# Kernel tuning notes

Measured on AMD Instinct MI355X. Metric: run time of the kernel, lower is better.

## Reference

```python
import jax, jax.numpy as jnp
import numpy as np

L = 32            # fixed label space replacing torch.unique (labels in [0, L))
DELTA_AGG = 0.5
DELTA_DIS = 1.5
REG_W = 0.001


def safe_norm(sq):
    # sqrt with zero-safe gradient: returns 0 where sq == 0
    safe = jnp.where(sq > 0, sq, 1.0)
    return jnp.where(sq > 0, jnp.sqrt(safe), 0.0)


def _single(emb, instance, kernel, training_mask):
    D = emb.shape[0]
    tm = training_mask > 0.5
    kn = kernel > 0.5
    inst = jnp.where(tm, instance, 0).reshape(-1)          # (N,) masked instance labels
    inst_k = jnp.where(tm & kn, instance, 0).reshape(-1)   # (N,) kernel-region labels
    embf = emb.reshape(D, -1).T                            # (N, D)
    ones = jnp.ones(inst.shape, dtype=jnp.float32)

    # per-label kernel means (emb_mean), label 0 stays zero as in torch
    cnt_k = jax.ops.segment_sum(ones, inst_k, num_segments=L)            # (L,)
    sum_k = jax.ops.segment_sum(embf, inst_k, num_segments=L)            # (L, D)
    emb_mean = sum_k / jnp.maximum(cnt_k, 1.0)[:, None]
    emb_mean = emb_mean.at[0].set(0.0)

    present = cnt_k > 0
    num_instance = jnp.sum(present.astype(jnp.int32))
    nz = present & (jnp.arange(L) > 0)

    # aggregation loss: per-pixel distance to own instance's kernel mean
    diff = embf - emb_mean[inst]                                          # (N, D)
    dist = safe_norm(jnp.sum(diff * diff, axis=1))
    val = jnp.log(jax.nn.relu(dist - DELTA_AGG) ** 2 + 1.0)
    sum_v = jax.ops.segment_sum(val, inst, num_segments=L)
    cnt = jax.ops.segment_sum(ones, inst, num_segments=L)
    l_agg_per = sum_v / jnp.maximum(cnt, 1.0)
    l_agg = jnp.sum(jnp.where(nz, l_agg_per, 0.0)) / jnp.maximum(num_instance - 1, 1)

    # discrimination loss: all pairs of distinct non-background present labels
    pdiff = emb_mean[:, None, :] - emb_mean[None, :, :]                   # (L, L, D)
    pdist = safe_norm(jnp.sum(pdiff * pdiff, axis=-1))
    pval = jnp.log(jax.nn.relu(2.0 * DELTA_DIS - pdist) ** 2 + 1.0)
    pmask = nz[:, None] & nz[None, :] & ~jnp.eye(L, dtype=bool)
    n_pairs = jnp.sum(pmask.astype(jnp.float32))
    l_dis = jnp.sum(jnp.where(pmask, pval, 0.0)) / jnp.maximum(n_pairs, 1.0)
    l_dis = jnp.where(num_instance > 2, l_dis, 0.0)

    # regularizer over the num_instance present columns of emb_mean
    reg = jnp.log(safe_norm(jnp.sum(emb_mean * emb_mean, axis=1)) + 1.0)
    l_reg = jnp.sum(jnp.where(present, reg, 0.0)) / jnp.maximum(num_instance, 1) * REG_W

    loss = l_agg + l_dis + l_reg
    return jnp.where(num_instance <= 1, 0.0, loss)


def setup_inputs() -> dict:
    key = jax.random.key(0)
    k1, k2, k3, k4 = jax.random.split(key, 4)
    B, D, H, W = 8, 4, 736, 736
    emb = jax.random.normal(k1, (B, D, H, W), dtype=jnp.float32)
    instance = jax.random.randint(k2, (B, H, W), 0, L, dtype=jnp.int32)
    kernel = jax.random.uniform(k3, (B, H, W), dtype=jnp.float32)
    training_mask = jax.random.uniform(k4, (B, H, W), dtype=jnp.float32)
    return {"emb": emb, "instance": instance, "kernel": kernel, "training_mask": training_mask}


def reference(emb, instance, kernel, training_mask):
    return jax.vmap(_single)(emb, instance, kernel, training_mask)
```

## Files before the change

### kernel.cpp

```cpp
#include <hip/hip_runtime.h>

#define LBL 32
#define NPIX (736 * 736)
#define NQ (NPIX / 4)
#define QPB 512
#define NBA 265
#define BATCH 8
#define DELTA_AGG 0.5f
#define DELTA_DIS 1.5f
#define REG_W 0.001f

#define LAB_BASE 0
#define PA_BASE (BATCH * NQ)
#define RED_BASE (PA_BASE + BATCH * NBA * 192)
#define PC_BASE (RED_BASE + BATCH * 256)

__device__ __forceinline__ unsigned int procQuad(
    const int4 iv, const float4 kv, const float4 mv,
    const float4 e0, const float4 e1, const float4 e2, const float4 e3,
    float* __restrict__ s_cnt, float* __restrict__ s_sum,
    float* __restrict__ s_cta, bool& has0) {
  const int labs[4] = {iv.x, iv.y, iv.z, iv.w};
  const float ks[4] = {kv.x, kv.y, kv.z, kv.w};
  const float ms[4] = {mv.x, mv.y, mv.z, mv.w};
  const float c0[4] = {e0.x, e0.y, e0.z, e0.w};
  const float c1[4] = {e1.x, e1.y, e1.z, e1.w};
  const float c2[4] = {e2.x, e2.y, e2.z, e2.w};
  const float c3[4] = {e3.x, e3.y, e3.z, e3.w};
  unsigned int labw = 0;
#pragma unroll
  for (int j = 0; j < 4; j++) {
    const bool m = ms[j] > 0.5f;
    const int li = m ? labs[j] : 0;
    const bool kf = m && (ks[j] > 0.5f);
    labw |= ((unsigned int)li) << (8 * j);
    if (li > 0) {
      atomicAdd(&s_cta[li], 1.0f);
      if (kf) {
        atomicAdd(&s_cnt[li], 1.0f);
        atomicAdd(&s_sum[0 * 33 + li], c0[j]);
        atomicAdd(&s_sum[1 * 33 + li], c1[j]);
        atomicAdd(&s_sum[2 * 33 + li], c2[j]);
        atomicAdd(&s_sum[3 * 33 + li], c3[j]);
      } else {
        has0 = true;
      }
    } else {
      has0 = true;
    }
  }
  return labw;
}

__global__ __launch_bounds__(256) void kA(
    const float* __restrict__ emb, const int* __restrict__ inst,
    const float* __restrict__ kern, const float* __restrict__ mask,
    float* __restrict__ ws) {
  const int b = blockIdx.y;
  const int t = threadIdx.x;
  __shared__ float s_cnt[LBL];
  __shared__ float s_sum[4 * 33];
  __shared__ float s_cta[LBL];
  if (t < LBL) { s_cnt[t] = 0.f; s_cta[t] = 0.f; }
  if (t < 4 * 33) s_sum[t] = 0.f;
  __syncthreads();

  const long base = (long)b * NPIX;
  const float* ebase = emb + (long)b * 4 * NPIX;
  const int4* ip = (const int4*)(inst + base);
  const float4* kp = (const float4*)(kern + base);
  const float4* mp = (const float4*)(mask + base);
  const float4* p0 = (const float4*)(ebase);
  const float4* p1 = (const float4*)(ebase + NPIX);
  const float4* p2 = (const float4*)(ebase + 2 * NPIX);
  const float4* p3 = (const float4*)(ebase + 3 * NPIX);

  const int q0 = blockIdx.x * QPB + t;
  const int q1 = q0 + 256;
  const bool v1 = (q1 < NQ);

  const int4 iva = ip[q0];
  const float4 kva = kp[q0], mva = mp[q0];
  const float4 ea0 = p0[q0], ea1 = p1[q0], ea2 = p2[q0], ea3 = p3[q0];
  int4 ivb;
  float4 kvb, mvb, fb0, fb1, fb2, fb3;
  if (v1) {
    ivb = ip[q1]; kvb = kp[q1]; mvb = mp[q1];
    fb0 = p0[q1]; fb1 = p1[q1]; fb2 = p2[q1]; fb3 = p3[q1];
  }

  bool has0 = false;
  unsigned int* labp = (unsigned int*)(ws + LAB_BASE) + (size_t)b * NQ;

  labp[q0] = procQuad(iva, kva, mva, ea0, ea1, ea2, ea3,
                      s_cnt, s_sum, s_cta, has0);
  if (v1) {
    labp[q1] = procQuad(ivb, kvb, mvb, fb0, fb1, fb2, fb3,
                        s_cnt, s_sum, s_cta, has0);
  }

  if (has0) s_cnt[0] = 1.0f;
  __syncthreads();
  float* po = ws + PA_BASE + ((size_t)b * NBA + blockIdx.x) * 192;
  if (t < 192) {
    float v;
    if (t < 32) v = s_cnt[t];
    else if (t < 160) {
      const int e = t - 32;
      v = s_sum[(e & 3) * 33 + (e >> 2)];
    } else {
      v = s_cta[t - 160];
    }
    po[t] = v;
  }
}

__global__ __launch_bounds__(256) void kB(float* __restrict__ ws) {
  const int b = blockIdx.y;
  const int col = blockIdx.x * 4 + (threadIdx.x >> 6);
  const int lane = threadIdx.x & 63;
  const float* pa = ws + PA_BASE + (size_t)b * NBA * 192 + col;
  float s = 0.f;
  for (int g = lane; g < NBA; g += 64) s += pa[(size_t)g * 192];
#pragma unroll
  for (int o = 32; o > 0; o >>= 1) s += __shfl_down(s, o);
  if (lane == 0) ws[RED_BASE + b * 256 + col] = s;
}

__device__ __forceinline__ void aggQuad(const unsigned int lw,
    const float4 e0, const float4 e1, const float4 e2, const float4 e3,
    const float* __restrict__ s_mean, float* __restrict__ s_val) {
  const float c0[4] = {e0.x, e0.y, e0.z, e0.w};
  const float c1[4] = {e1.x, e1.y, e1.z, e1.w};
  const float c2[4] = {e2.x, e2.y, e2.z, e2.w};
  const float c3[4] = {e3.x, e3.y, e3.z, e3.w};
#pragma unroll
  for (int j = 0; j < 4; j++) {
    const int li = (lw >> (8 * j)) & 0xFF;
    if (li > 0) {
      const float d0 = c0[j] - s_mean[li * 4 + 0];
      const float d1 = c1[j] - s_mean[li * 4 + 1];
      const float d2 = c2[j] - s_mean[li * 4 + 2];
      const float d3 = c3[j] - s_mean[li * 4 + 3];
      const float sq = d0 * d0 + d1 * d1 + d2 * d2 + d3 * d3;
      const float dist = (sq > 0.f) ? sqrtf(sq) : 0.f;
      const float tt = fmaxf(dist - DELTA_AGG, 0.f);
      atomicAdd(&s_val[li], logf(fmaf(tt, tt, 1.0f)));
    }
  }
}

__global__ __launch_bounds__(256) void kC(const float* __restrict__ emb,
                                          float* __restrict__ ws) {
  const int b = blockIdx.y;
  const int t = threadIdx.x;
  __shared__ float s_mean[LBL * 4];
  __shared__ float s_val[LBL];
  const float* rd = ws + RED_BASE + b * 256;
  if (t < LBL * 4) {
    const int l = t >> 2;
    s_mean[t] = (l == 0) ? 0.f : rd[32 + t] / fmaxf(rd[l], 1.0f);
  }
  if (t < LBL) s_val[t] = 0.f;
  __syncthreads();

  const unsigned int* labp = (const unsigned int*)(ws + LAB_BASE) + (size_t)b * NQ;
  const float* ebase = emb + (long)b * 4 * NPIX;
  const float4* p0 = (const float4*)(ebase);
  const float4* p1 = (const float4*)(ebase + NPIX);
  const float4* p2 = (const float4*)(ebase + 2 * NPIX);
  const float4* p3 = (const float4*)(ebase + 3 * NPIX);
  const int q0 = blockIdx.x * QPB + t;
  const int q1 = q0 + 256;
  const bool v1 = (q1 < NQ);

  const unsigned int lwa = labp[q0];
  const float4 ea0 = p0[q0], ea1 = p1[q0], ea2 = p2[q0], ea3 = p3[q0];
  unsigned int lwb = 0;
  float4 fb0, fb1, fb2, fb3;
  if (v1) {
    lwb = labp[q1];
    fb0 = p0[q1]; fb1 = p1[q1]; fb2 = p2[q1]; fb3 = p3[q1];
  }

  aggQuad(lwa, ea0, ea1, ea2, ea3, s_mean, s_val);
  if (v1) aggQuad(lwb, fb0, fb1, fb2, fb3, s_mean, s_val);

  __syncthreads();
  float* po = ws + PC_BASE + ((size_t)b * NBA + blockIdx.x) * 32;
  if (t < 32) po[t] = s_val[t];
}

__global__ __launch_bounds__(1024) void kD(const float* __restrict__ ws,
                                           float* __restrict__ out) {
  const int b = blockIdx.x;
  const int t = threadIdx.x;
  const int col = t >> 5, sub = t & 31;
  const float* pc = ws + PC_BASE + (size_t)b * NBA * 32 + col;
  float s = 0.f;
  for (int g = sub; g < NBA; g += 32) s += pc[(size_t)g * 32];
  __shared__ float red[LBL][33];
  red[col][sub] = s;

  const float* rd = ws + RED_BASE + b * 256;
  __shared__ float sm[LBL * 4];
  __shared__ float scc[LBL];
  __shared__ float sca[LBL];
  if (t >= 512 && t < 640) {
    const int e = t - 512, l = e >> 2;
    sm[e] = (l == 0) ? 0.f : rd[32 + e] / fmaxf(rd[l], 1.0f);
  } else if (t >= 640 && t < 672) {
    scc[t - 640] = rd[t - 640];
  } else if (t >= 672 && t < 704) {
    sca[t - 672] = rd[160 + (t - 672)];
  }
  __syncthreads();
  __shared__ float sv[LBL];
  if (t < 32) {
    float v = 0.f;
#pragma unroll
    for (int k = 0; k < 32; k++) v += red[t][k];
    sv[t] = v;
  }
  __syncthreads();

  if (t < 64) {
    const int lane = t;
    const bool pres = (lane < LBL) && (scc[lane & 31] > 0.f);
    const unsigned long long bal_p = __ballot(pres);
    const int num_instance = __popcll(bal_p);
    const bool nz = pres && (lane > 0);
    const unsigned long long bal_nz = __ballot(nz);

    float agg = 0.f;
    if (nz) agg = sv[lane] / fmaxf(sca[lane], 1.0f);

    float reg = 0.f;
    if (pres) {
      float sq = 0.f;
#pragma unroll
      for (int d = 0; d < 4; d++) sq += sm[lane * 4 + d] * sm[lane * 4 + d];
      const float nrm = (sq > 0.f) ? sqrtf(sq) : 0.f;
      reg = logf(nrm + 1.0f);
    }

    float dis = 0.f, npair = 0.f;
    for (int pi = lane; pi < LBL * LBL; pi += 64) {
      const int i = pi >> 5, j = pi & 31;
      if (i != j && ((bal_nz >> i) & 1ull) && ((bal_nz >> j) & 1ull)) {
        float sq = 0.f;
#pragma unroll
        for (int d = 0; d < 4; d++) {
          const float df = sm[i * 4 + d] - sm[j * 4 + d];
          sq += df * df;
        }
        const float pdist = (sq > 0.f) ? sqrtf(sq) : 0.f;
        const float tt = fmaxf(2.0f * DELTA_DIS - pdist, 0.f);
        dis += logf(fmaf(tt, tt, 1.0f));
        npair += 1.0f;
      }
    }

#pragma unroll
    for (int o = 32; o > 0; o >>= 1) {
      agg += __shfl_down(agg, o);
      reg += __shfl_down(reg, o);
      dis += __shfl_down(dis, o);
      npair += __shfl_down(npair, o);
    }

    if (lane == 0) {
      const float l_agg = agg / fmaxf((float)(num_instance - 1), 1.0f);
      const float l_dis = (num_instance > 2) ? dis / fmaxf(npair, 1.0f) : 0.f;
      const float l_reg = reg / fmaxf((float)num_instance, 1.0f) * REG_W;
      const float loss = l_agg + l_dis + l_reg;
      out[b] = (num_instance <= 1) ? 0.f : loss;
    }
  }
}

extern "C" void kernel_launch(void* const* d_in, const int* in_sizes, int n_in,
                              void* d_out, int out_size, void* d_ws,
                              size_t ws_size, hipStream_t stream) {
  const float* emb = (const float*)d_in[0];
  const int* instance = (const int*)d_in[1];
  const float* kern = (const float*)d_in[2];
  const float* mask = (const float*)d_in[3];
  float* out = (float*)d_out;
  float* ws = (float*)d_ws;

  dim3 gridA(NBA, BATCH);
  kA<<<gridA, 256, 0, stream>>>(emb, instance, kern, mask, ws);
  dim3 gridB(48, BATCH);
  kB<<<gridB, 256, 0, stream>>>(ws);
  kC<<<gridA, 256, 0, stream>>>(emb, ws);
  kD<<<BATCH, 1024, 0, stream>>>(ws, out);
}
```

Measured before the change: 186.4 us.

## Fuse four kernels into one cooperative kernel keeping embeddings in registers as bf16

Replaces the four-kernel pipeline with a single cooperative kernel on a persistent 96x8 grid. Grid-wide syncs separate the histogram, reduction, aggregation and final-loss phases. Each thread keeps its pixels' labels and bf16-packed embeddings in registers, so the second pass does not re-read emb from global memory and the packed label buffer is no longer written. The costs are three grid barriers, fewer blocks with heavier per-thread work and register pressure, and bf16 rounding in the aggregation distances, which changes numerics slightly. If the cooperative launch fails, the old four-kernel path runs instead.

```diff
diff --git a/kernel.cpp b/kernel.cpp
--- a/kernel.cpp
+++ b/kernel.cpp
@@ -1,19 +1,273 @@
 #include <hip/hip_runtime.h>
+#include <hip/hip_cooperative_groups.h>
+
+namespace cg = cooperative_groups;
 
 #define LBL 32
 #define NPIX (736 * 736)
 #define NQ (NPIX / 4)
-#define QPB 512
-#define NBA 265
+#define NGRP 529
 #define BATCH 8
 #define DELTA_AGG 0.5f
 #define DELTA_DIS 1.5f
 #define REG_W 0.001f
 
+#define QPB 512
+#define NBA 265
 #define LAB_BASE 0
 #define PA_BASE (BATCH * NQ)
 #define RED_BASE (PA_BASE + BATCH * NBA * 192)
 #define PC_BASE (RED_BASE + BATCH * 256)
+
+#define QPT 6
+#define NBB 96
+#define FPA_BASE 1600000
+#define FRED_BASE (FPA_BASE + BATCH * NBB * 192)
+#define FPC_BASE (FRED_BASE + BATCH * 256)
+
+__device__ __forceinline__ unsigned short f2bf(float f) {
+  unsigned int u = __float_as_uint(f);
+  unsigned int r = u + 0x7FFFu + ((u >> 16) & 1u);
+  return (unsigned short)(r >> 16);
+}
+__device__ __forceinline__ float bfl(unsigned int w) {
+  return __uint_as_float(w << 16);
+}
+__device__ __forceinline__ float bfh(unsigned int w) {
+  return __uint_as_float(w & 0xFFFF0000u);
+}
+
+__global__ __launch_bounds__(256, 3) void kF(
+    const float* __restrict__ emb, const int* __restrict__ inst,
+    const float* __restrict__ kern, const float* __restrict__ mask,
+    float* __restrict__ ws, float* __restrict__ out) {
+  const int bx = blockIdx.x;
+  const int by = blockIdx.y;
+  const int t = threadIdx.x;
+
+  __shared__ float s_cnt[LBL];
+  __shared__ float s_sum[4 * 33];
+  __shared__ float s_cta[LBL];
+  __shared__ float s_mean[LBL * 4];
+  __shared__ float s_val[LBL];
+  __shared__ float redl[LBL][9];
+  __shared__ float sv[LBL];
+
+  if (t < LBL) { s_cnt[t] = 0.f; s_cta[t] = 0.f; }
+  if (t < 4 * 33) s_sum[t] = 0.f;
+  __syncthreads();
+
+  const long base = (long)by * NPIX;
+  const float* ebase = emb + (long)by * 4 * NPIX;
+  const int4* ip = (const int4*)(inst + base);
+  const float4* kp = (const float4*)(kern + base);
+  const float4* mp = (const float4*)(mask + base);
+  const float4* p0 = (const float4*)(ebase);
+  const float4* p1 = (const float4*)(ebase + NPIX);
+  const float4* p2 = (const float4*)(ebase + 2 * NPIX);
+  const float4* p3 = (const float4*)(ebase + 3 * NPIX);
+
+  uint2 pk[QPT][4];
+  unsigned int labw[QPT];
+  bool has0 = false;
+
+#pragma unroll
+  for (int k = 0; k < QPT; k++) {
+    const int grp = bx * QPT + k;
+    if (grp < NGRP) {
+      const int q = grp * 256 + t;
+      const int4 iv = ip[q];
+      const float4 kv = kp[q], mv = mp[q];
+      const float4 e0 = p0[q], e1 = p1[q], e2 = p2[q], e3 = p3[q];
+      const int labs[4] = {iv.x, iv.y, iv.z, iv.w};
+      const float ks[4] = {kv.x, kv.y, kv.z, kv.w};
+      const float ms[4] = {mv.x, mv.y, mv.z, mv.w};
+      const float c0[4] = {e0.x, e0.y, e0.z, e0.w};
+      const float c1[4] = {e1.x, e1.y, e1.z, e1.w};
+      const float c2[4] = {e2.x, e2.y, e2.z, e2.w};
+      const float c3[4] = {e3.x, e3.y, e3.z, e3.w};
+      unsigned int lw = 0;
+#pragma unroll
+      for (int j = 0; j < 4; j++) {
+        const bool m = ms[j] > 0.5f;
+        const int li = m ? labs[j] : 0;
+        const bool kf = m && (ks[j] > 0.5f);
+        lw |= ((unsigned int)li) << (8 * j);
+        pk[k][j].x = ((unsigned int)f2bf(c0[j])) |
+                     (((unsigned int)f2bf(c1[j])) << 16);
+        pk[k][j].y = ((unsigned int)f2bf(c2[j])) |
+                     (((unsigned int)f2bf(c3[j])) << 16);
+        if (li > 0) {
+          atomicAdd(&s_cta[li], 1.0f);
+          if (kf) {
+            atomicAdd(&s_cnt[li], 1.0f);
+            atomicAdd(&s_sum[0 * 33 + li], c0[j]);
+            atomicAdd(&s_sum[1 * 33 + li], c1[j]);
+            atomicAdd(&s_sum[2 * 33 + li], c2[j]);
+            atomicAdd(&s_sum[3 * 33 + li], c3[j]);
+          } else has0 = true;
+        } else has0 = true;
+      }
+      labw[k] = lw;
+    } else {
+      labw[k] = 0;
+    }
+  }
+
+  if (has0) s_cnt[0] = 1.0f;
+  __syncthreads();
+  {
+    float* po = ws + FPA_BASE + ((size_t)by * NBB + bx) * 192;
+    if (t < 192) {
+      float v;
+      if (t < 32) v = s_cnt[t];
+      else if (t < 160) {
+        const int e = t - 32;
+        v = s_sum[(e & 3) * 33 + (e >> 2)];
+      } else {
+        v = s_cta[t - 160];
+      }
+      po[t] = v;
+    }
+  }
+
+  __threadfence();
+  cg::this_grid().sync();
+
+  {
+    const int gw = ((by * NBB + bx) << 2) + (t >> 6);
+    const int lane = t & 63;
+    if (gw < BATCH * 192) {
+      const int b = gw / 192, col = gw - b * 192;
+      const float* pa = ws + FPA_BASE + (size_t)b * NBB * 192 + col;
+      float s = 0.f;
+      for (int g = lane; g < NBB; g += 64) s += pa[(size_t)g * 192];
+#pragma unroll
+      for (int o = 32; o > 0; o >>= 1) s += __shfl_down(s, o);
+      if (lane == 0) ws[FRED_BASE + b * 256 + col] = s;
+    }
+  }
+
+  __threadfence();
+  cg::this_grid().sync();
+
+  {
+    const float* rd = ws + FRED_BASE + by * 256;
+    if (t < LBL * 4) {
+      const int l = t >> 2;
+      s_mean[t] = (l == 0) ? 0.f : rd[32 + t] / fmaxf(rd[l], 1.0f);
+    }
+    if (t < LBL) s_val[t] = 0.f;
+    __syncthreads();
+
+#pragma unroll
+    for (int k = 0; k < QPT; k++) {
+      const int grp = bx * QPT + k;
+      if (grp < NGRP) {
+#pragma unroll
+        for (int j = 0; j < 4; j++) {
+          const int li = (labw[k] >> (8 * j)) & 0xFF;
+          if (li > 0) {
+            const float d0 = bfl(pk[k][j].x) - s_mean[li * 4 + 0];
+            const float d1 = bfh(pk[k][j].x) - s_mean[li * 4 + 1];
+            const float d2 = bfl(pk[k][j].y) - s_mean[li * 4 + 2];
+            const float d3 = bfh(pk[k][j].y) - s_mean[li * 4 + 3];
+            const float sq = d0 * d0 + d1 * d1 + d2 * d2 + d3 * d3;
+            const float dist = (sq > 0.f) ? sqrtf(sq) : 0.f;
+            const float tt = fmaxf(dist - DELTA_AGG, 0.f);
+            atomicAdd(&s_val[li], logf(fmaf(tt, tt, 1.0f)));
+          }
+        }
+      }
+    }
+    __syncthreads();
+    if (t < 32) ws[FPC_BASE + ((size_t)by * NBB + bx) * 32 + t] = s_val[t];
+  }
+
+  __threadfence();
+  cg::this_grid().sync();
+
+  if (by == 0 && bx < BATCH) {
+    const int b2 = bx;
+    const int col = t >> 3, sub = t & 7;
+    const float* pc = ws + FPC_BASE + (size_t)b2 * NBB * 32 + col;
+    float s = 0.f;
+    for (int g = sub; g < NBB; g += 8) s += pc[(size_t)g * 32];
+    redl[col][sub] = s;
+
+    const float* rd2 = ws + FRED_BASE + b2 * 256;
+    if (t < 128) {
+      const int l = t >> 2;
+      s_mean[t] = (l == 0) ? 0.f : rd2[32 + t] / fmaxf(rd2[l], 1.0f);
+    } else if (t < 160) {
+      s_cnt[t - 128] = rd2[t - 128];
+    } else if (t < 192) {
+      s_cta[t - 160] = rd2[160 + (t - 160)];
+    }
+    __syncthreads();
+    if (t < 32) {
+      float v = 0.f;
+#pragma unroll
+      for (int k2 = 0; k2 < 8; k2++) v += redl[t][k2];
+      sv[t] = v;
+    }
+    __syncthreads();
+
+    if (t < 64) {
+      const int lane = t;
+      const bool pres = (lane < LBL) && (s_cnt[lane & 31] > 0.f);
+      const unsigned long long bal_p = __ballot(pres);
+      const int num_instance = __popcll(bal_p);
+      const bool nz = pres && (lane > 0);
+      const unsigned long long bal_nz = __ballot(nz);
+
+      float agg = 0.f;
+      if (nz) agg = sv[lane] / fmaxf(s_cta[lane], 1.0f);
+
+      float reg = 0.f;
+      if (pres) {
+        float sq = 0.f;
+#pragma unroll
+        for (int d = 0; d < 4; d++) sq += s_mean[lane * 4 + d] * s_mean[lane * 4 + d];
+        const float nrm = (sq > 0.f) ? sqrtf(sq) : 0.f;
+        reg = logf(nrm + 1.0f);
+      }
+
+      float dis = 0.f, npair = 0.f;
+      for (int pi = lane; pi < LBL * LBL; pi += 64) {
+        const int i = pi >> 5, j = pi & 31;
+        if (i != j && ((bal_nz >> i) & 1ull) && ((bal_nz >> j) & 1ull)) {
+          float sq = 0.f;
+#pragma unroll
+          for (int d = 0; d < 4; d++) {
+            const float df = s_mean[i * 4 + d] - s_mean[j * 4 + d];
+            sq += df * df;
+          }
+          const float pdist = (sq > 0.f) ? sqrtf(sq) : 0.f;
+          const float tt = fmaxf(2.0f * DELTA_DIS - pdist, 0.f);
+          dis += logf(fmaf(tt, tt, 1.0f));
+          npair += 1.0f;
+        }
+      }
+
+#pragma unroll
+      for (int o = 32; o > 0; o >>= 1) {
+        agg += __shfl_down(agg, o);
+        reg += __shfl_down(reg, o);
+        dis += __shfl_down(dis, o);
+        npair += __shfl_down(npair, o);
+      }
+
+      if (lane == 0) {
+        const float l_agg = agg / fmaxf((float)(num_instance - 1), 1.0f);
+        const float l_dis = (num_instance > 2) ? dis / fmaxf(npair, 1.0f) : 0.f;
+        const float l_reg = reg / fmaxf((float)num_instance, 1.0f) * REG_W;
+        const float loss = l_agg + l_dis + l_reg;
+        out[b2] = (num_instance <= 1) ? 0.f : loss;
+      }
+    }
+  }
+}
 
 __device__ __forceinline__ unsigned int procQuad(
     const int4 iv, const float4 kv, const float4 mv,
@@ -42,12 +296,8 @@
         atomicAdd(&s_sum[1 * 33 + li], c1[j]);
         atomicAdd(&s_sum[2 * 33 + li], c2[j]);
         atomicAdd(&s_sum[3 * 33 + li], c3[j]);
-      } else {
-        has0 = true;
-      }
-    } else {
-      has0 = true;
-    }
+      } else has0 = true;
+    } else has0 = true;
   }
   return labw;
 }
@@ -91,13 +341,9 @@
 
   bool has0 = false;
   unsigned int* labp = (unsigned int*)(ws + LAB_BASE) + (size_t)b * NQ;
-
-  labp[q0] = procQuad(iva, kva, mva, ea0, ea1, ea2, ea3,
-                      s_cnt, s_sum, s_cta, has0);
-  if (v1) {
-    labp[q1] = procQuad(ivb, kvb, mvb, fb0, fb1, fb2, fb3,
-                        s_cnt, s_sum, s_cta, has0);
-  }
+  labp[q0] = procQuad(iva, kva, mva, ea0, ea1, ea2, ea3, s_cnt, s_sum, s_cta, has0);
+  if (v1)
+    labp[q1] = procQuad(ivb, kvb, mvb, fb0, fb1, fb2, fb3, s_cnt, s_sum, s_cta, has0);
 
   if (has0) s_cnt[0] = 1.0f;
   __syncthreads();
@@ -108,9 +354,7 @@
     else if (t < 160) {
       const int e = t - 32;
       v = s_sum[(e & 3) * 33 + (e >> 2)];
-    } else {
-      v = s_cta[t - 160];
-    }
+    } else v = s_cta[t - 160];
     po[t] = v;
   }
 }
@@ -127,7 +371,7 @@
   if (lane == 0) ws[RED_BASE + b * 256 + col] = s;
 }
 
-__device__ __forceinline__ void aggQuad(const unsigned int lw,
+__device__ __forceinline__ void aggQuadF(const unsigned int lw,
     const float4 e0, const float4 e1, const float4 e2, const float4 e3,
     const float* __restrict__ s_mean, float* __restrict__ s_val) {
   const float c0[4] = {e0.x, e0.y, e0.z, e0.w};
@@ -183,8 +427,8 @@
     fb0 = p0[q1]; fb1 = p1[q1]; fb2 = p2[q1]; fb3 = p3[q1];
   }
 
-  aggQuad(lwa, ea0, ea1, ea2, ea3, s_mean, s_val);
-  if (v1) aggQuad(lwb, fb0, fb1, fb2, fb3, s_mean, s_val);
+  aggQuadF(lwa, ea0, ea1, ea2, ea3, s_mean, s_val);
+  if (v1) aggQuadF(lwb, fb0, fb1, fb2, fb3, s_mean, s_val);
 
   __syncthreads();
   float* po = ws + PC_BASE + ((size_t)b * NBA + blockIdx.x) * 32;
@@ -289,10 +533,18 @@
   float* out = (float*)d_out;
   float* ws = (float*)d_ws;
 
-  dim3 gridA(NBA, BATCH);
-  kA<<<gridA, 256, 0, stream>>>(emb, instance, kern, mask, ws);
-  dim3 gridB(48, BATCH);
-  kB<<<gridB, 256, 0, stream>>>(ws);
-  kC<<<gridA, 256, 0, stream>>>(emb, ws);
-  kD<<<BATCH, 1024, 0, stream>>>(ws, out);
-}
+  dim3 grid(NBB, BATCH);
+  dim3 block(256);
+  void* args[] = {(void*)&emb, (void*)&instance, (void*)&kern,
+                  (void*)&mask, (void*)&ws,      (void*)&out};
+  hipError_t rc =
+      hipLaunchCooperativeKernel((void*)kF, grid, block, args, 0, stream);
+  if (rc != hipSuccess) {
+    dim3 gridA(NBA, BATCH);
+    kA<<<gridA, 256, 0, stream>>>(emb, instance, kern, mask, ws);
+    dim3 gridB(48, BATCH);
+    kB<<<gridB, 256, 0, stream>>>(ws);
+    kC<<<gridA, 256, 0, stream>>>(emb, ws);
+    kD<<<BATCH, 1024, 0, stream>>>(ws, out);
+  }
+}
```

Measured after the change: 665.9 us. +257.2%, slower.
